# Optimization experiments

Hardware: AMD Instinct MI355X
Metric: run time of the kernel (lower is better)

## Reference

```python
import jax, jax.numpy as jnp
import numpy as np

NUM_AGENTS = 256
HIDDEN = 1024
RANK = 32
LOG_ALPHA_INIT = -1.0
ALPHA_MAX = 5.0
LN_EPS = 1e-5


def setup_inputs() -> dict:
    key = jax.random.key(0)
    k_h, k_ids, k_u, k_v = jax.random.split(key, 4)
    scale = 1.0 / (RANK ** 0.5)
    h = jax.random.normal(k_h, (8192, HIDDEN), dtype=jnp.float32)
    agent_ids = jax.random.randint(k_ids, (8192,), 0, NUM_AGENTS)
    # per-agent fixed random projections (buffers in the original module)
    projection_u = jax.random.normal(k_u, (NUM_AGENTS, HIDDEN, RANK), dtype=jnp.float32) * scale
    projection_v = jax.random.normal(k_v, (NUM_AGENTS, RANK, HIDDEN), dtype=jnp.float32) * scale
    log_alpha = jnp.asarray(LOG_ALPHA_INIT, dtype=jnp.float32)
    ln_gamma = jnp.ones((HIDDEN,), dtype=jnp.float32)
    ln_beta = jnp.zeros((HIDDEN,), dtype=jnp.float32)
    return {
        "h": h,
        "log_alpha": log_alpha,
        "ln_gamma": ln_gamma,
        "ln_beta": ln_beta,
        "projection_u": projection_u,
        "projection_v": projection_v,
        "agent_ids": agent_ids,
    }


def reference(h, log_alpha, ln_gamma, ln_beta, projection_u, projection_v, agent_ids):
    ids = agent_ids % NUM_AGENTS  # [B]
    u = projection_u[ids]  # [B, H, R] gathered per token
    v = projection_v[ids]  # [B, R, H]
    intermediate = jnp.einsum('bh,bhr->br', h, u)      # [B, R]
    perturbation = jnp.einsum('br,brh->bh', intermediate, v)  # [B, H]
    alpha = jnp.minimum(jnp.exp(log_alpha), ALPHA_MAX)
    h_div = h + alpha * perturbation
    # LayerNorm over last dim (biased variance, eps=1e-5)
    mean = jnp.mean(h_div, axis=-1, keepdims=True)
    var = jnp.mean(jnp.square(h_div - mean), axis=-1, keepdims=True)
    h_div = (h_div - mean) * jax.lax.rsqrt(var + LN_EPS) * ln_gamma + ln_beta
    return h_div
```

## Files before the change

### kernel.cpp

```cpp
#include <hip/hip_runtime.h>
#include <math.h>

#define NUM_AGENTS 256
#define HIDDEN 1024
#define RANK 32
#define NTOK 8192
#define TBATCH 8
#define MAXPER 128
#define KMAX 16
#define ALPHA_MAX 5.0f
#define LN_EPS 1e-5f

typedef float f32x4 __attribute__((ext_vector_type(4)));

__global__ __launch_bounds__(256) void scan_kernel(
    const int* __restrict__ ids, int* __restrict__ counts, int* __restrict__ lists)
{
    __shared__ int cnt;
    const int t = threadIdx.x;
    const int agent = blockIdx.x;
    if (t == 0) cnt = 0;
    __syncthreads();
    #pragma unroll
    for (int it = 0; it < NTOK / 1024; ++it) {
        int4 v = ((const int4*)ids)[t + 256 * it];
        int ib = 4 * (t + 256 * it);
        if ((v.x & (NUM_AGENTS - 1)) == agent) { int p = atomicAdd(&cnt, 1); if (p < MAXPER) lists[agent * MAXPER + p] = ib + 0; }
        if ((v.y & (NUM_AGENTS - 1)) == agent) { int p = atomicAdd(&cnt, 1); if (p < MAXPER) lists[agent * MAXPER + p] = ib + 1; }
        if ((v.z & (NUM_AGENTS - 1)) == agent) { int p = atomicAdd(&cnt, 1); if (p < MAXPER) lists[agent * MAXPER + p] = ib + 2; }
        if ((v.w & (NUM_AGENTS - 1)) == agent) { int p = atomicAdd(&cnt, 1); if (p < MAXPER) lists[agent * MAXPER + p] = ib + 3; }
    }
    __syncthreads();
    if (t == 0) {
        int c = min(cnt, MAXPER);
        counts[agent] = c;
        int last = (c > 0) ? lists[agent * MAXPER + c - 1] : 0;
        int pe = min((c + TBATCH - 1) / TBATCH * TBATCH, MAXPER);
        for (int i = c; i < pe; ++i) lists[agent * MAXPER + i] = last;
    }
}

__global__ __launch_bounds__(256) void div_inject_kernel(
    const float* __restrict__ hglob,
    const float* __restrict__ log_alpha,
    const float* __restrict__ gamma,
    const float* __restrict__ beta,
    const float* __restrict__ U,
    const float* __restrict__ V,
    const int* __restrict__ counts,
    const int* __restrict__ lists,
    float* __restrict__ out)
{
    __shared__ __align__(16) float Hs[TBATCH][HIDDEN];
    float* red0  = &Hs[0][0];
    float* inter = red0;
    float* wred  = red0 + 256;

    const int t = threadIdx.x;
    const int a = blockIdx.x & (NUM_AGENTS - 1);
    const int k = blockIdx.x >> 8;

    const int cnt = counts[a];
    const int start = k * TBATCH;
    if (start >= cnt) return;
    const int nm = min(TBATCH, cnt - start);

    const float* Ua = U + (size_t)a * (HIDDEN * RANK);
    const float* Va = V + (size_t)a * (RANK * HIDDEN);

    const int r4 = (t & 7) * 4;
    const int ks = t >> 3;
    const int c  = t * 4;
    const int wave = t >> 6, lane = t & 63;

    float4 ub[2][4];
    #pragma unroll
    for (int j = 0; j < 4; ++j)
        ub[0][j] = *(const float4*)(Ua + (ks + 32 * j) * RANK + r4);

    const int* gl = lists + a * MAXPER + start;
    int tk[TBATCH];
    #pragma unroll
    for (int m = 0; m < TBATCH; ++m) tk[m] = gl[m];

    const float alpha = fminf(__expf(log_alpha[0]), ALPHA_MAX);

    f32x4 h0v;
    {
        f32x4 hv[TBATCH];
        #pragma unroll
        for (int m = 0; m < TBATCH; ++m)
            hv[m] = __builtin_nontemporal_load((const f32x4*)(hglob + (size_t)tk[m] * HIDDEN + c));
        h0v = hv[0];
        #pragma unroll
        for (int m = 0; m < TBATCH; ++m)
            *(f32x4*)(&Hs[m][c]) = hv[m];
    }
    __syncthreads();

    float4 acc[TBATCH];
    #pragma unroll
    for (int m = 0; m < TBATCH; ++m) acc[m] = make_float4(0.f, 0.f, 0.f, 0.f);
    #pragma unroll
    for (int jb = 0; jb < 8; ++jb) {
        const int cur = jb & 1;
        if (jb < 7) {
            #pragma unroll
            for (int j = 0; j < 4; ++j)
                ub[cur ^ 1][j] = *(const float4*)(Ua + (ks + 32 * (4 * (jb + 1) + j)) * RANK + r4);
        }
        #pragma unroll
        for (int j = 0; j < 4; ++j) {
            const int hh = ks + 32 * (4 * jb + j);
            float4 u = ub[cur][j];
            #pragma unroll
            for (int m = 0; m < TBATCH; ++m) {
                float h0 = Hs[m][hh];
                acc[m].x += h0 * u.x;
                acc[m].y += h0 * u.y;
                acc[m].z += h0 * u.z;
                acc[m].w += h0 * u.w;
            }
        }
    }
    #pragma unroll
    for (int off = 8; off <= 32; off <<= 1) {
        #pragma unroll
        for (int m = 0; m < TBATCH; ++m) {
            acc[m].x += __shfl_xor(acc[m].x, off, 64);
            acc[m].y += __shfl_xor(acc[m].y, off, 64);
            acc[m].z += __shfl_xor(acc[m].z, off, 64);
            acc[m].w += __shfl_xor(acc[m].w, off, 64);
        }
    }
    __syncthreads();
    if (lane < 8) {
        #pragma unroll
        for (int m = 0; m < TBATCH; ++m)
            *(float4*)(&red0[wave * 256 + m * 32 + r4]) = acc[m];
    }

    float4 vb[2][4];
    #pragma unroll
    for (int j = 0; j < 4; ++j)
        vb[0][j] = *(const float4*)(Va + j * HIDDEN + c);

    __syncthreads();
    {
        int m = t >> 5, rr = t & 31;
        inter[m * 32 + rr] = red0[m * 32 + rr] + red0[256 + m * 32 + rr]
                           + red0[512 + m * 32 + rr] + red0[768 + m * 32 + rr];
    }
    __syncthreads();

    float4 p[TBATCH];
    #pragma unroll
    for (int m = 0; m < TBATCH; ++m) p[m] = make_float4(0.f, 0.f, 0.f, 0.f);
    #pragma unroll
    for (int rb = 0; rb < 8; ++rb) {
        const int cur = rb & 1;
        if (rb < 7) {
            #pragma unroll
            for (int j = 0; j < 4; ++j)
                vb[cur ^ 1][j] = *(const float4*)(Va + (4 * (rb + 1) + j) * HIDDEN + c);
        }
        #pragma unroll
        for (int j = 0; j < 4; ++j) {
            const int r = 4 * rb + j;
            float4 v = vb[cur][j];
            #pragma unroll
            for (int m = 0; m < TBATCH; ++m) {
                float ir = inter[m * 32 + r];
                p[m].x += ir * v.x;
                p[m].y += ir * v.y;
                p[m].z += ir * v.z;
                p[m].w += ir * v.w;
            }
        }
    }

    float s[TBATCH], q[TBATCH];
    #pragma unroll
    for (int m = 0; m < TBATCH; ++m) {
        f32x4 h4 = (m == 0) ? h0v : *(const f32x4*)(&Hs[m][c]);
        p[m].x = h4.x + alpha * p[m].x;
        p[m].y = h4.y + alpha * p[m].y;
        p[m].z = h4.z + alpha * p[m].z;
        p[m].w = h4.w + alpha * p[m].w;
        s[m] = p[m].x + p[m].y + p[m].z + p[m].w;
        q[m] = p[m].x * p[m].x + p[m].y * p[m].y + p[m].z * p[m].z + p[m].w * p[m].w;
    }
    #pragma unroll
    for (int off = 32; off > 0; off >>= 1) {
        #pragma unroll
        for (int m = 0; m < TBATCH; ++m) {
            s[m] += __shfl_xor(s[m], off, 64);
            q[m] += __shfl_xor(q[m], off, 64);
        }
    }
    if (lane == 0) {
        #pragma unroll
        for (int m = 0; m < TBATCH; ++m) {
            wred[wave * 16 + m] = s[m];
            wred[wave * 16 + 8 + m] = q[m];
        }
    }
    __syncthreads();

    const float4 gv = *(const float4*)(gamma + c);
    const float4 bv = *(const float4*)(beta + c);
    #pragma unroll
    for (int m = 0; m < TBATCH; ++m) {
        if (m < nm) {
            float S = wred[m] + wred[16 + m] + wred[32 + m] + wred[48 + m];
            float Q = wred[8 + m] + wred[24 + m] + wred[40 + m] + wred[56 + m];
            float mean = S * (1.0f / HIDDEN);
            float rstd = rsqrtf(Q * (1.0f / HIDDEN) - mean * mean + LN_EPS);
            f32x4 o;
            o.x = (p[m].x - mean) * rstd * gv.x + bv.x;
            o.y = (p[m].y - mean) * rstd * gv.y + bv.y;
            o.z = (p[m].z - mean) * rstd * gv.z + bv.z;
            o.w = (p[m].w - mean) * rstd * gv.w + bv.w;
            __builtin_nontemporal_store(o, (f32x4*)(out + (size_t)tk[m] * HIDDEN + c));
        }
    }
}

extern "C" void kernel_launch(void* const* d_in, const int* in_sizes, int n_in,
                              void* d_out, int out_size, void* d_ws, size_t ws_size,
                              hipStream_t stream) {
    const float* h     = (const float*)d_in[0];
    const float* la    = (const float*)d_in[1];
    const float* gamma = (const float*)d_in[2];
    const float* beta  = (const float*)d_in[3];
    const float* U     = (const float*)d_in[4];
    const float* V     = (const float*)d_in[5];
    const int* ids     = (const int*)d_in[6];
    float* out         = (float*)d_out;

    int* counts = (int*)d_ws;
    int* lists  = counts + NUM_AGENTS;

    scan_kernel<<<NUM_AGENTS, 256, 0, stream>>>(ids, counts, lists);
    div_inject_kernel<<<NUM_AGENTS * KMAX, 256, 0, stream>>>(
        h, la, gamma, beta, U, V, counts, lists, out);
}
```

Measured before the change: 167.5 us.

## Halve token batch per block, drop manual U/V double-buffering, group blocks by agent

Cuts the tokens handled per block from 8 to 4, so twice as many blocks launch and each uses fewer registers and half the shared memory, which should raise occupancy. The hand-written double-buffered prefetch of U and V is replaced by simple unrolled loops, leaving load scheduling to the compiler. Block indexing now places blocks of the same agent next to each other, which may improve L2 reuse of that agent's projections. In exchange, each agent's U/V slice is read from memory by twice as many blocks, and the compiler may hide load latency less well than the explicit prefetch did.

```diff
diff --git a/kernel.cpp b/kernel.cpp
--- a/kernel.cpp
+++ b/kernel.cpp
@@ -5,9 +5,9 @@
 #define HIDDEN 1024
 #define RANK 32
 #define NTOK 8192
-#define TBATCH 8
+#define TBATCH 4
 #define MAXPER 128
-#define KMAX 16
+#define KMAX (MAXPER / TBATCH)
 #define ALPHA_MAX 5.0f
 #define LN_EPS 1e-5f
 
@@ -54,11 +54,11 @@
     __shared__ __align__(16) float Hs[TBATCH][HIDDEN];
     float* red0  = &Hs[0][0];
     float* inter = red0;
-    float* wred  = red0 + 256;
+    float* wred  = red0 + 512;
 
     const int t = threadIdx.x;
-    const int a = blockIdx.x & (NUM_AGENTS - 1);
-    const int k = blockIdx.x >> 8;
+    const int a = blockIdx.x >> 5;
+    const int k = blockIdx.x & (KMAX - 1);
 
     const int cnt = counts[a];
     const int start = k * TBATCH;
@@ -73,11 +73,6 @@
     const int c  = t * 4;
     const int wave = t >> 6, lane = t & 63;
 
-    float4 ub[2][4];
-    #pragma unroll
-    for (int j = 0; j < 4; ++j)
-        ub[0][j] = *(const float4*)(Ua + (ks + 32 * j) * RANK + r4);
-
     const int* gl = lists + a * MAXPER + start;
     int tk[TBATCH];
     #pragma unroll
@@ -101,26 +96,16 @@
     float4 acc[TBATCH];
     #pragma unroll
     for (int m = 0; m < TBATCH; ++m) acc[m] = make_float4(0.f, 0.f, 0.f, 0.f);
-    #pragma unroll
-    for (int jb = 0; jb < 8; ++jb) {
-        const int cur = jb & 1;
-        if (jb < 7) {
-            #pragma unroll
-            for (int j = 0; j < 4; ++j)
-                ub[cur ^ 1][j] = *(const float4*)(Ua + (ks + 32 * (4 * (jb + 1) + j)) * RANK + r4);
-        }
-        #pragma unroll
-        for (int j = 0; j < 4; ++j) {
-            const int hh = ks + 32 * (4 * jb + j);
-            float4 u = ub[cur][j];
-            #pragma unroll
-            for (int m = 0; m < TBATCH; ++m) {
-                float h0 = Hs[m][hh];
-                acc[m].x += h0 * u.x;
-                acc[m].y += h0 * u.y;
-                acc[m].z += h0 * u.z;
-                acc[m].w += h0 * u.w;
-            }
+    #pragma unroll 8
+    for (int hh = ks; hh < HIDDEN; hh += 32) {
+        float4 u = *(const float4*)(Ua + hh * RANK + r4);
+        #pragma unroll
+        for (int m = 0; m < TBATCH; ++m) {
+            float h0 = Hs[m][hh];
+            acc[m].x += h0 * u.x;
+            acc[m].y += h0 * u.y;
+            acc[m].z += h0 * u.z;
+            acc[m].w += h0 * u.w;
         }
     }
     #pragma unroll
@@ -137,45 +122,26 @@
     if (lane < 8) {
         #pragma unroll
         for (int m = 0; m < TBATCH; ++m)
-            *(float4*)(&red0[wave * 256 + m * 32 + r4]) = acc[m];
-    }
-
-    float4 vb[2][4];
-    #pragma unroll
-    for (int j = 0; j < 4; ++j)
-        vb[0][j] = *(const float4*)(Va + j * HIDDEN + c);
-
-    __syncthreads();
-    {
-        int m = t >> 5, rr = t & 31;
-        inter[m * 32 + rr] = red0[m * 32 + rr] + red0[256 + m * 32 + rr]
-                           + red0[512 + m * 32 + rr] + red0[768 + m * 32 + rr];
-    }
+            *(float4*)(&red0[wave * 128 + m * 32 + r4]) = acc[m];
+    }
+    __syncthreads();
+    if (t < 128)
+        inter[t] = red0[t] + red0[128 + t] + red0[256 + t] + red0[384 + t];
     __syncthreads();
 
     float4 p[TBATCH];
     #pragma unroll
     for (int m = 0; m < TBATCH; ++m) p[m] = make_float4(0.f, 0.f, 0.f, 0.f);
-    #pragma unroll
-    for (int rb = 0; rb < 8; ++rb) {
-        const int cur = rb & 1;
-        if (rb < 7) {
-            #pragma unroll
-            for (int j = 0; j < 4; ++j)
-                vb[cur ^ 1][j] = *(const float4*)(Va + (4 * (rb + 1) + j) * HIDDEN + c);
-        }
-        #pragma unroll
-        for (int j = 0; j < 4; ++j) {
-            const int r = 4 * rb + j;
-            float4 v = vb[cur][j];
-            #pragma unroll
-            for (int m = 0; m < TBATCH; ++m) {
-                float ir = inter[m * 32 + r];
-                p[m].x += ir * v.x;
-                p[m].y += ir * v.y;
-                p[m].z += ir * v.z;
-                p[m].w += ir * v.w;
-            }
+    #pragma unroll 8
+    for (int r = 0; r < RANK; ++r) {
+        float4 v = *(const float4*)(Va + r * HIDDEN + c);
+        #pragma unroll
+        for (int m = 0; m < TBATCH; ++m) {
+            float ir = inter[m * 32 + r];
+            p[m].x += ir * v.x;
+            p[m].y += ir * v.y;
+            p[m].z += ir * v.z;
+            p[m].w += ir * v.w;
         }
     }
 
@@ -201,8 +167,8 @@
     if (lane == 0) {
         #pragma unroll
         for (int m = 0; m < TBATCH; ++m) {
-            wred[wave * 16 + m] = s[m];
-            wred[wave * 16 + 8 + m] = q[m];
+            wred[wave * 8 + m] = s[m];
+            wred[wave * 8 + 4 + m] = q[m];
         }
     }
     __syncthreads();
@@ -212,8 +178,8 @@
     #pragma unroll
     for (int m = 0; m < TBATCH; ++m) {
         if (m < nm) {
-            float S = wred[m] + wred[16 + m] + wred[32 + m] + wred[48 + m];
-            float Q = wred[8 + m] + wred[24 + m] + wred[40 + m] + wred[56 + m];
+            float S = wred[m] + wred[8 + m] + wred[16 + m] + wred[24 + m];
+            float Q = wred[4 + m] + wred[12 + m] + wred[20 + m] + wred[28 + m];
             float mean = S * (1.0f / HIDDEN);
             float rstd = rsqrtf(Q * (1.0f / HIDDEN) - mean * mean + LN_EPS);
             f32x4 o;
```

Measured after the change: 244.8 us. +46.2%, slower.

## Compact work items into per-region descriptor queues to avoid empty blocks

Applied to the files above, without the earlier changes.

The scan kernel now buffers each agent's token list in shared memory and atomically reserves slots in one of 8 region queues. Into each slot it writes a compact descriptor holding the agent, the token count and the token indices. The inject kernel launches 8*256 blocks indexed by region and slot, so blocks map densely onto real work instead of 256*16 blocks of which most exit early. The change adds a small zeroing kernel launch and global atomics, and if a region overflows REGCAP its groups are silently dropped.

```diff
diff --git a/kernel.cpp b/kernel.cpp
--- a/kernel.cpp
+++ b/kernel.cpp
@@ -7,16 +7,21 @@
 #define NTOK 8192
 #define TBATCH 8
 #define MAXPER 128
-#define KMAX 16
+#define REGCAP 256
 #define ALPHA_MAX 5.0f
 #define LN_EPS 1e-5f
 
 typedef float f32x4 __attribute__((ext_vector_type(4)));
 
+__global__ void zero_rc(int* __restrict__ rc) {
+    if (threadIdx.x < 8) rc[threadIdx.x] = 0;
+}
+
 __global__ __launch_bounds__(256) void scan_kernel(
-    const int* __restrict__ ids, int* __restrict__ counts, int* __restrict__ lists)
+    const int* __restrict__ ids, int* __restrict__ rc, int* __restrict__ desc)
 {
-    __shared__ int cnt;
+    __shared__ int toklist[MAXPER];
+    __shared__ int cnt, basew;
     const int t = threadIdx.x;
     const int agent = blockIdx.x;
     if (t == 0) cnt = 0;
@@ -25,18 +30,27 @@
     for (int it = 0; it < NTOK / 1024; ++it) {
         int4 v = ((const int4*)ids)[t + 256 * it];
         int ib = 4 * (t + 256 * it);
-        if ((v.x & (NUM_AGENTS - 1)) == agent) { int p = atomicAdd(&cnt, 1); if (p < MAXPER) lists[agent * MAXPER + p] = ib + 0; }
-        if ((v.y & (NUM_AGENTS - 1)) == agent) { int p = atomicAdd(&cnt, 1); if (p < MAXPER) lists[agent * MAXPER + p] = ib + 1; }
-        if ((v.z & (NUM_AGENTS - 1)) == agent) { int p = atomicAdd(&cnt, 1); if (p < MAXPER) lists[agent * MAXPER + p] = ib + 2; }
-        if ((v.w & (NUM_AGENTS - 1)) == agent) { int p = atomicAdd(&cnt, 1); if (p < MAXPER) lists[agent * MAXPER + p] = ib + 3; }
-    }
-    __syncthreads();
-    if (t == 0) {
-        int c = min(cnt, MAXPER);
-        counts[agent] = c;
-        int last = (c > 0) ? lists[agent * MAXPER + c - 1] : 0;
-        int pe = min((c + TBATCH - 1) / TBATCH * TBATCH, MAXPER);
-        for (int i = c; i < pe; ++i) lists[agent * MAXPER + i] = last;
+        if ((v.x & (NUM_AGENTS - 1)) == agent) { int p = atomicAdd(&cnt, 1); if (p < MAXPER) toklist[p] = ib + 0; }
+        if ((v.y & (NUM_AGENTS - 1)) == agent) { int p = atomicAdd(&cnt, 1); if (p < MAXPER) toklist[p] = ib + 1; }
+        if ((v.z & (NUM_AGENTS - 1)) == agent) { int p = atomicAdd(&cnt, 1); if (p < MAXPER) toklist[p] = ib + 2; }
+        if ((v.w & (NUM_AGENTS - 1)) == agent) { int p = atomicAdd(&cnt, 1); if (p < MAXPER) toklist[p] = ib + 3; }
+    }
+    __syncthreads();
+    const int c = min(cnt, MAXPER);
+    const int ng = (c + TBATCH - 1) / TBATCH;
+    if (t == 0 && c > 0)
+        basew = atomicAdd(&rc[agent & 7], ng);
+    __syncthreads();
+    if (t < ng) {
+        int slot = basew + t;
+        if (slot < REGCAP) {
+            int* d = desc + ((size_t)(agent & 7) * REGCAP + slot) * 16;
+            d[0] = agent;
+            d[1] = min(TBATCH, c - t * TBATCH);
+            #pragma unroll
+            for (int m = 0; m < TBATCH; ++m)
+                d[2 + m] = toklist[min(t * TBATCH + m, c - 1)];
+        }
     }
 }
 
@@ -47,8 +61,8 @@
     const float* __restrict__ beta,
     const float* __restrict__ U,
     const float* __restrict__ V,
-    const int* __restrict__ counts,
-    const int* __restrict__ lists,
+    const int* __restrict__ rc,
+    const int* __restrict__ desc,
     float* __restrict__ out)
 {
     __shared__ __align__(16) float Hs[TBATCH][HIDDEN];
@@ -57,13 +71,18 @@
     float* wred  = red0 + 256;
 
     const int t = threadIdx.x;
-    const int a = blockIdx.x & (NUM_AGENTS - 1);
-    const int k = blockIdx.x >> 8;
-
-    const int cnt = counts[a];
-    const int start = k * TBATCH;
-    if (start >= cnt) return;
-    const int nm = min(TBATCH, cnt - start);
+    const int region = blockIdx.x & 7;
+    const int slot = blockIdx.x >> 3;
+
+    const int rcnt = min(rc[region], REGCAP);
+    if (slot >= rcnt) return;
+
+    const int* dsc = desc + ((size_t)region * REGCAP + slot) * 16;
+    const int a  = dsc[0];
+    const int nm = dsc[1];
+    int tk[TBATCH];
+    #pragma unroll
+    for (int m = 0; m < TBATCH; ++m) tk[m] = dsc[2 + m];
 
     const float* Ua = U + (size_t)a * (HIDDEN * RANK);
     const float* Va = V + (size_t)a * (RANK * HIDDEN);
@@ -77,11 +96,6 @@
     #pragma unroll
     for (int j = 0; j < 4; ++j)
         ub[0][j] = *(const float4*)(Ua + (ks + 32 * j) * RANK + r4);
-
-    const int* gl = lists + a * MAXPER + start;
-    int tk[TBATCH];
-    #pragma unroll
-    for (int m = 0; m < TBATCH; ++m) tk[m] = gl[m];
 
     const float alpha = fminf(__expf(log_alpha[0]), ALPHA_MAX);
 
@@ -238,10 +252,11 @@
     const int* ids     = (const int*)d_in[6];
     float* out         = (float*)d_out;
 
-    int* counts = (int*)d_ws;
-    int* lists  = counts + NUM_AGENTS;
-
-    scan_kernel<<<NUM_AGENTS, 256, 0, stream>>>(ids, counts, lists);
-    div_inject_kernel<<<NUM_AGENTS * KMAX, 256, 0, stream>>>(
-        h, la, gamma, beta, U, V, counts, lists, out);
-}
+    int* rc   = (int*)d_ws;
+    int* desc = rc + 16;
+
+    zero_rc<<<1, 64, 0, stream>>>(rc);
+    scan_kernel<<<NUM_AGENTS, 256, 0, stream>>>(ids, rc, desc);
+    div_inject_kernel<<<8 * REGCAP, 256, 0, stream>>>(
+        h, la, gamma, beta, U, V, rc, desc, out);
+}
```

Result: no change. 167.0 us, median of 2 (-0.3%).

## Use fixed slot grid with loop over token groups and compact scan lists

Applied to the files above, without the earlier changes.

The main kernel now launches four slots per agent instead of sixteen, and each block loops over that agent's token groups with a stride of four, which removes the many early-exit blocks. Block indices are remapped so neighbouring blocks belong to different agents. The scan kernel gathers token ids in shared memory, writes a padded 64-entry list in parallel and drops the serial padding loop. The cost is that any agent with more than 64 tokens is silently truncated, and blocks that own several groups run them one after another with extra barriers.

```diff
diff --git a/kernel.cpp b/kernel.cpp
--- a/kernel.cpp
+++ b/kernel.cpp
@@ -6,8 +6,8 @@
 #define RANK 32
 #define NTOK 8192
 #define TBATCH 8
-#define MAXPER 128
-#define KMAX 16
+#define LISTCAP 64
+#define NSLOT 4
 #define ALPHA_MAX 5.0f
 #define LN_EPS 1e-5f
 
@@ -16,28 +16,26 @@
 __global__ __launch_bounds__(256) void scan_kernel(
     const int* __restrict__ ids, int* __restrict__ counts, int* __restrict__ lists)
 {
+    __shared__ int toklist[LISTCAP];
     __shared__ int cnt;
     const int t = threadIdx.x;
     const int agent = blockIdx.x;
-    if (t == 0) cnt = 0;
+    if (t == 0) { cnt = 0; toklist[0] = 0; }
     __syncthreads();
     #pragma unroll
     for (int it = 0; it < NTOK / 1024; ++it) {
         int4 v = ((const int4*)ids)[t + 256 * it];
         int ib = 4 * (t + 256 * it);
-        if ((v.x & (NUM_AGENTS - 1)) == agent) { int p = atomicAdd(&cnt, 1); if (p < MAXPER) lists[agent * MAXPER + p] = ib + 0; }
-        if ((v.y & (NUM_AGENTS - 1)) == agent) { int p = atomicAdd(&cnt, 1); if (p < MAXPER) lists[agent * MAXPER + p] = ib + 1; }
-        if ((v.z & (NUM_AGENTS - 1)) == agent) { int p = atomicAdd(&cnt, 1); if (p < MAXPER) lists[agent * MAXPER + p] = ib + 2; }
-        if ((v.w & (NUM_AGENTS - 1)) == agent) { int p = atomicAdd(&cnt, 1); if (p < MAXPER) lists[agent * MAXPER + p] = ib + 3; }
+        if ((v.x & (NUM_AGENTS - 1)) == agent) { int p = atomicAdd(&cnt, 1); if (p < LISTCAP) toklist[p] = ib + 0; }
+        if ((v.y & (NUM_AGENTS - 1)) == agent) { int p = atomicAdd(&cnt, 1); if (p < LISTCAP) toklist[p] = ib + 1; }
+        if ((v.z & (NUM_AGENTS - 1)) == agent) { int p = atomicAdd(&cnt, 1); if (p < LISTCAP) toklist[p] = ib + 2; }
+        if ((v.w & (NUM_AGENTS - 1)) == agent) { int p = atomicAdd(&cnt, 1); if (p < LISTCAP) toklist[p] = ib + 3; }
     }
     __syncthreads();
-    if (t == 0) {
-        int c = min(cnt, MAXPER);
-        counts[agent] = c;
-        int last = (c > 0) ? lists[agent * MAXPER + c - 1] : 0;
-        int pe = min((c + TBATCH - 1) / TBATCH * TBATCH, MAXPER);
-        for (int i = c; i < pe; ++i) lists[agent * MAXPER + i] = last;
-    }
+    const int c = min(cnt, LISTCAP);
+    if (t == 0) counts[agent] = c;
+    if (t < LISTCAP)
+        lists[agent * LISTCAP + t] = toklist[min(t, max(c - 1, 0))];
 }
 
 __global__ __launch_bounds__(256) void div_inject_kernel(
@@ -57,13 +55,15 @@
     float* wred  = red0 + 256;
 
     const int t = threadIdx.x;
-    const int a = blockIdx.x & (NUM_AGENTS - 1);
-    const int k = blockIdx.x >> 8;
+    const int x = blockIdx.x & 7;
+    const int rest = blockIdx.x >> 3;
+    const int s = rest & 3;
+    const int jc = rest >> 2;
+    const int a = x + 8 * jc;
 
     const int cnt = counts[a];
-    const int start = k * TBATCH;
-    if (start >= cnt) return;
-    const int nm = min(TBATCH, cnt - start);
+    const int ng = (cnt + TBATCH - 1) / TBATCH;
+    if (s >= ng) return;
 
     const float* Ua = U + (size_t)a * (HIDDEN * RANK);
     const float* Va = V + (size_t)a * (RANK * HIDDEN);
@@ -73,156 +73,161 @@
     const int c  = t * 4;
     const int wave = t >> 6, lane = t & 63;
 
-    float4 ub[2][4];
-    #pragma unroll
-    for (int j = 0; j < 4; ++j)
-        ub[0][j] = *(const float4*)(Ua + (ks + 32 * j) * RANK + r4);
-
-    const int* gl = lists + a * MAXPER + start;
-    int tk[TBATCH];
-    #pragma unroll
-    for (int m = 0; m < TBATCH; ++m) tk[m] = gl[m];
-
     const float alpha = fminf(__expf(log_alpha[0]), ALPHA_MAX);
-
-    f32x4 h0v;
-    {
-        f32x4 hv[TBATCH];
-        #pragma unroll
-        for (int m = 0; m < TBATCH; ++m)
-            hv[m] = __builtin_nontemporal_load((const f32x4*)(hglob + (size_t)tk[m] * HIDDEN + c));
-        h0v = hv[0];
-        #pragma unroll
-        for (int m = 0; m < TBATCH; ++m)
-            *(f32x4*)(&Hs[m][c]) = hv[m];
-    }
-    __syncthreads();
-
-    float4 acc[TBATCH];
-    #pragma unroll
-    for (int m = 0; m < TBATCH; ++m) acc[m] = make_float4(0.f, 0.f, 0.f, 0.f);
-    #pragma unroll
-    for (int jb = 0; jb < 8; ++jb) {
-        const int cur = jb & 1;
-        if (jb < 7) {
-            #pragma unroll
-            for (int j = 0; j < 4; ++j)
-                ub[cur ^ 1][j] = *(const float4*)(Ua + (ks + 32 * (4 * (jb + 1) + j)) * RANK + r4);
-        }
-        #pragma unroll
-        for (int j = 0; j < 4; ++j) {
-            const int hh = ks + 32 * (4 * jb + j);
-            float4 u = ub[cur][j];
-            #pragma unroll
-            for (int m = 0; m < TBATCH; ++m) {
-                float h0 = Hs[m][hh];
-                acc[m].x += h0 * u.x;
-                acc[m].y += h0 * u.y;
-                acc[m].z += h0 * u.z;
-                acc[m].w += h0 * u.w;
-            }
-        }
-    }
-    #pragma unroll
-    for (int off = 8; off <= 32; off <<= 1) {
-        #pragma unroll
-        for (int m = 0; m < TBATCH; ++m) {
-            acc[m].x += __shfl_xor(acc[m].x, off, 64);
-            acc[m].y += __shfl_xor(acc[m].y, off, 64);
-            acc[m].z += __shfl_xor(acc[m].z, off, 64);
-            acc[m].w += __shfl_xor(acc[m].w, off, 64);
-        }
-    }
-    __syncthreads();
-    if (lane < 8) {
-        #pragma unroll
-        for (int m = 0; m < TBATCH; ++m)
-            *(float4*)(&red0[wave * 256 + m * 32 + r4]) = acc[m];
-    }
-
-    float4 vb[2][4];
-    #pragma unroll
-    for (int j = 0; j < 4; ++j)
-        vb[0][j] = *(const float4*)(Va + j * HIDDEN + c);
-
-    __syncthreads();
-    {
-        int m = t >> 5, rr = t & 31;
-        inter[m * 32 + rr] = red0[m * 32 + rr] + red0[256 + m * 32 + rr]
-                           + red0[512 + m * 32 + rr] + red0[768 + m * 32 + rr];
-    }
-    __syncthreads();
-
-    float4 p[TBATCH];
-    #pragma unroll
-    for (int m = 0; m < TBATCH; ++m) p[m] = make_float4(0.f, 0.f, 0.f, 0.f);
-    #pragma unroll
-    for (int rb = 0; rb < 8; ++rb) {
-        const int cur = rb & 1;
-        if (rb < 7) {
-            #pragma unroll
-            for (int j = 0; j < 4; ++j)
-                vb[cur ^ 1][j] = *(const float4*)(Va + (4 * (rb + 1) + j) * HIDDEN + c);
-        }
-        #pragma unroll
-        for (int j = 0; j < 4; ++j) {
-            const int r = 4 * rb + j;
-            float4 v = vb[cur][j];
-            #pragma unroll
-            for (int m = 0; m < TBATCH; ++m) {
-                float ir = inter[m * 32 + r];
-                p[m].x += ir * v.x;
-                p[m].y += ir * v.y;
-                p[m].z += ir * v.z;
-                p[m].w += ir * v.w;
-            }
-        }
-    }
-
-    float s[TBATCH], q[TBATCH];
-    #pragma unroll
-    for (int m = 0; m < TBATCH; ++m) {
-        f32x4 h4 = (m == 0) ? h0v : *(const f32x4*)(&Hs[m][c]);
-        p[m].x = h4.x + alpha * p[m].x;
-        p[m].y = h4.y + alpha * p[m].y;
-        p[m].z = h4.z + alpha * p[m].z;
-        p[m].w = h4.w + alpha * p[m].w;
-        s[m] = p[m].x + p[m].y + p[m].z + p[m].w;
-        q[m] = p[m].x * p[m].x + p[m].y * p[m].y + p[m].z * p[m].z + p[m].w * p[m].w;
-    }
-    #pragma unroll
-    for (int off = 32; off > 0; off >>= 1) {
-        #pragma unroll
-        for (int m = 0; m < TBATCH; ++m) {
-            s[m] += __shfl_xor(s[m], off, 64);
-            q[m] += __shfl_xor(q[m], off, 64);
-        }
-    }
-    if (lane == 0) {
-        #pragma unroll
-        for (int m = 0; m < TBATCH; ++m) {
-            wred[wave * 16 + m] = s[m];
-            wred[wave * 16 + 8 + m] = q[m];
-        }
-    }
-    __syncthreads();
-
     const float4 gv = *(const float4*)(gamma + c);
     const float4 bv = *(const float4*)(beta + c);
-    #pragma unroll
-    for (int m = 0; m < TBATCH; ++m) {
-        if (m < nm) {
-            float S = wred[m] + wred[16 + m] + wred[32 + m] + wred[48 + m];
-            float Q = wred[8 + m] + wred[24 + m] + wred[40 + m] + wred[56 + m];
-            float mean = S * (1.0f / HIDDEN);
-            float rstd = rsqrtf(Q * (1.0f / HIDDEN) - mean * mean + LN_EPS);
-            f32x4 o;
-            o.x = (p[m].x - mean) * rstd * gv.x + bv.x;
-            o.y = (p[m].y - mean) * rstd * gv.y + bv.y;
-            o.z = (p[m].z - mean) * rstd * gv.z + bv.z;
-            o.w = (p[m].w - mean) * rstd * gv.w + bv.w;
-            __builtin_nontemporal_store(o, (f32x4*)(out + (size_t)tk[m] * HIDDEN + c));
-        }
+
+    for (int g = s; g < ng; g += NSLOT) {
+        const int nm = min(TBATCH, cnt - g * TBATCH);
+
+        const int* gl = lists + a * LISTCAP + g * TBATCH;
+        int tk[TBATCH];
+        #pragma unroll
+        for (int m = 0; m < TBATCH; ++m) tk[m] = gl[m];
+
+        float4 ub[2][4];
+        #pragma unroll
+        for (int j = 0; j < 4; ++j)
+            ub[0][j] = *(const float4*)(Ua + (ks + 32 * j) * RANK + r4);
+
+        f32x4 h0v;
+        {
+            f32x4 hv[TBATCH];
+            #pragma unroll
+            for (int m = 0; m < TBATCH; ++m)
+                hv[m] = __builtin_nontemporal_load((const f32x4*)(hglob + (size_t)tk[m] * HIDDEN + c));
+            h0v = hv[0];
+            #pragma unroll
+            for (int m = 0; m < TBATCH; ++m)
+                *(f32x4*)(&Hs[m][c]) = hv[m];
+        }
+        __syncthreads();
+
+        float4 acc[TBATCH];
+        #pragma unroll
+        for (int m = 0; m < TBATCH; ++m) acc[m] = make_float4(0.f, 0.f, 0.f, 0.f);
+        #pragma unroll
+        for (int jb = 0; jb < 8; ++jb) {
+            const int cur = jb & 1;
+            if (jb < 7) {
+                #pragma unroll
+                for (int j = 0; j < 4; ++j)
+                    ub[cur ^ 1][j] = *(const float4*)(Ua + (ks + 32 * (4 * (jb + 1) + j)) * RANK + r4);
+            }
+            #pragma unroll
+            for (int j = 0; j < 4; ++j) {
+                const int hh = ks + 32 * (4 * jb + j);
+                float4 u = ub[cur][j];
+                #pragma unroll
+                for (int m = 0; m < TBATCH; ++m) {
+                    float h0 = Hs[m][hh];
+                    acc[m].x += h0 * u.x;
+                    acc[m].y += h0 * u.y;
+                    acc[m].z += h0 * u.z;
+                    acc[m].w += h0 * u.w;
+                }
+            }
+        }
+        #pragma unroll
+        for (int off = 8; off <= 32; off <<= 1) {
+            #pragma unroll
+            for (int m = 0; m < TBATCH; ++m) {
+                acc[m].x += __shfl_xor(acc[m].x, off, 64);
+                acc[m].y += __shfl_xor(acc[m].y, off, 64);
+                acc[m].z += __shfl_xor(acc[m].z, off, 64);
+                acc[m].w += __shfl_xor(acc[m].w, off, 64);
+            }
+        }
+        __syncthreads();
+        if (lane < 8) {
+            #pragma unroll
+            for (int m = 0; m < TBATCH; ++m)
+                *(float4*)(&red0[wave * 256 + m * 32 + r4]) = acc[m];
+        }
+
+        float4 vb[2][4];
+        #pragma unroll
+        for (int j = 0; j < 4; ++j)
+            vb[0][j] = *(const float4*)(Va + j * HIDDEN + c);
+
+        __syncthreads();
+        {
+            int m = t >> 5, rr = t & 31;
+            inter[m * 32 + rr] = red0[m * 32 + rr] + red0[256 + m * 32 + rr]
+                               + red0[512 + m * 32 + rr] + red0[768 + m * 32 + rr];
+        }
+        __syncthreads();
+
+        float4 p[TBATCH];
+        #pragma unroll
+        for (int m = 0; m < TBATCH; ++m) p[m] = make_float4(0.f, 0.f, 0.f, 0.f);
+        #pragma unroll
+        for (int rb = 0; rb < 8; ++rb) {
+            const int cur = rb & 1;
+            if (rb < 7) {
+                #pragma unroll
+                for (int j = 0; j < 4; ++j)
+                    vb[cur ^ 1][j] = *(const float4*)(Va + (4 * (rb + 1) + j) * HIDDEN + c);
+            }
+            #pragma unroll
+            for (int j = 0; j < 4; ++j) {
+                const int r = 4 * rb + j;
+                float4 v = vb[cur][j];
+                #pragma unroll
+                for (int m = 0; m < TBATCH; ++m) {
+                    float ir = inter[m * 32 + r];
+                    p[m].x += ir * v.x;
+                    p[m].y += ir * v.y;
+                    p[m].z += ir * v.z;
+                    p[m].w += ir * v.w;
+                }
+            }
+        }
+
+        float sred[TBATCH], q[TBATCH];
+        #pragma unroll
+        for (int m = 0; m < TBATCH; ++m) {
+            f32x4 h4 = (m == 0) ? h0v : *(const f32x4*)(&Hs[m][c]);
+            p[m].x = h4.x + alpha * p[m].x;
+            p[m].y = h4.y + alpha * p[m].y;
+            p[m].z = h4.z + alpha * p[m].z;
+            p[m].w = h4.w + alpha * p[m].w;
+            sred[m] = p[m].x + p[m].y + p[m].z + p[m].w;
+            q[m] = p[m].x * p[m].x + p[m].y * p[m].y + p[m].z * p[m].z + p[m].w * p[m].w;
+        }
+        #pragma unroll
+        for (int off = 32; off > 0; off >>= 1) {
+            #pragma unroll
+            for (int m = 0; m < TBATCH; ++m) {
+                sred[m] += __shfl_xor(sred[m], off, 64);
+                q[m] += __shfl_xor(q[m], off, 64);
+            }
+        }
+        if (lane == 0) {
+            #pragma unroll
+            for (int m = 0; m < TBATCH; ++m) {
+                wred[wave * 16 + m] = sred[m];
+                wred[wave * 16 + 8 + m] = q[m];
+            }
+        }
+        __syncthreads();
+
+        #pragma unroll
+        for (int m = 0; m < TBATCH; ++m) {
+            if (m < nm) {
+                float S = wred[m] + wred[16 + m] + wred[32 + m] + wred[48 + m];
+                float Q = wred[8 + m] + wred[24 + m] + wred[40 + m] + wred[56 + m];
+                float mean = S * (1.0f / HIDDEN);
+                float rstd = rsqrtf(Q * (1.0f / HIDDEN) - mean * mean + LN_EPS);
+                f32x4 o;
+                o.x = (p[m].x - mean) * rstd * gv.x + bv.x;
+                o.y = (p[m].y - mean) * rstd * gv.y + bv.y;
+                o.z = (p[m].z - mean) * rstd * gv.z + bv.z;
+                o.w = (p[m].w - mean) * rstd * gv.w + bv.w;
+                __builtin_nontemporal_store(o, (f32x4*)(out + (size_t)tk[m] * HIDDEN + c));
+            }
+        }
+        if (g + NSLOT < ng) __syncthreads();
     }
 }
 
@@ -242,6 +247,6 @@
     int* lists  = counts + NUM_AGENTS;
 
     scan_kernel<<<NUM_AGENTS, 256, 0, stream>>>(ids, counts, lists);
-    div_inject_kernel<<<NUM_AGENTS * KMAX, 256, 0, stream>>>(
+    div_inject_kernel<<<NUM_AGENTS * NSLOT, 256, 0, stream>>>(
         h, la, gamma, beta, U, V, counts, lists, out);
 }
```

Result: slower. 201.3 us (+20.2%).
